# Kernel tuning notes

Hardware: AMD Instinct MI355X
Metric: run time of the kernel (lower is better)

The kernel has to match this reference:

```python
import jax, jax.numpy as jnp
import numpy as np

COUPLE_STRENGTH = 0.1
ITER_FISTA = 16
ITER_EIGENVAL = 20


def setup_inputs() -> dict:
    key = jax.random.key(0)
    k1, k2 = jax.random.split(key)
    # light field patches: (b, N, u, v, s, t, ch)
    x = jax.random.normal(k1, (8, 256, 5, 5, 4, 4, 3), dtype=jnp.float32)
    dim_signal = 5 * 5 * 4 * 4 * 3  # 1200
    dim_dict = 2 * dim_signal       # overcompleteness = 2 -> 2400
    D = jax.random.normal(k2, (dim_signal, dim_dict), dtype=jnp.float32)
    D = D / jnp.linalg.norm(D, axis=0, keepdims=True)  # UnitNorm(axis=0) constraint
    return {"x": x, "dictionary": D}


def _max_eigval(D):
    """von Mises power iteration for largest eigenvalue of D^T D."""
    v0 = jax.random.normal(jax.random.key(42), (D.shape[1],), dtype=D.dtype)
    v0 = v0 / jnp.linalg.norm(v0)

    def step(v, _):
        w = D.T @ (D @ v)
        n = jnp.linalg.norm(w)
        return w / n, n

    _, norms = jax.lax.scan(step, v0, None, length=ITER_EIGENVAL)
    return norms[-1]


def _soft_threshold(x, thr):
    return jnp.sign(x) * jnp.maximum(jnp.abs(x) - thr, 0.0)


def _sparse_code_fista(x2, D):
    """x2: (B, N, dim_signal); D: (dim_signal, dim_dict) -> codes (B, N, dim_dict)."""
    L = _max_eigval(D)            # Lipschitz constant of grad of 0.5*||Dz - x||^2
    thr = COUPLE_STRENGTH / L
    z0 = jnp.zeros(x2.shape[:-1] + (D.shape[1],), dtype=x2.dtype)
    carry0 = (z0, z0, jnp.float32(1.0))  # (z, y, t)

    def step(carry, _):
        z, y, t = carry
        recon = jnp.einsum('bnk,dk->bnd', y, D)             # (B,N,ds)
        grad = jnp.einsum('bnd,dk->bnk', recon - x2, D)     # (B,N,dd)
        z_new = _soft_threshold(y - grad / L, thr)
        t_new = 0.5 * (1.0 + jnp.sqrt(1.0 + 4.0 * t * t))
        y_new = z_new + ((t - 1.0) / t_new) * (z_new - z)   # Nesterov momentum
        return (z_new, y_new, t_new), None

    (z, _, _), _ = jax.lax.scan(step, carry0, None, length=ITER_FISTA)
    return z


def reference(x, dictionary):
    B, N, u, v, s, t, ch = x.shape
    x2 = x.reshape(B, N, u * v * s * t * ch)
    code = jax.lax.stop_gradient(_sparse_code_fista(x2, dictionary))
    recon = jnp.einsum('bnk,dk->bnd', code, dictionary)  # matmul(x, D, transpose_b=True)
    return recon.reshape(B, N, u, v, s, t, ch)
```

## Files before the change

kernel.cpp:

```cpp
#include <hip/hip_runtime.h>
#include <hip/hip_bf16.h>
#include <cmath>

#define DS 1200
#define DD 2400
#define MR 2048
#define KP 1216
#define NP1 1280
#define NG 2432
#define PPI 150

typedef __attribute__((ext_vector_type(8))) short s16x8;
typedef __attribute__((ext_vector_type(4))) float f32x4;

__device__ __forceinline__ float s2f(short s) {
    union { unsigned u; float f; } c;
    c.u = ((unsigned)(unsigned short)s) << 16;
    return c.f;
}
__device__ __forceinline__ short f2s(float f) {
    __hip_bfloat16 h = __float2bfloat16(f);
    return *reinterpret_cast<short*>(&h);
}
__device__ __forceinline__ float bf2f(__hip_bfloat16 h) { return __bfloat162float(h); }


__device__ __forceinline__ unsigned rotl32(unsigned x, int d) {
    return (x << d) | (x >> (32 - d));
}

__device__ void threefry2x32(unsigned k0, unsigned k1, unsigned x0, unsigned x1,
                             unsigned* o0, unsigned* o1) {
    unsigned ks0 = k0, ks1 = k1, ks2 = k0 ^ k1 ^ 0x1BD11BDAu;
    const int rotA[4] = {13, 15, 26, 6};
    const int rotB[4] = {17, 29, 16, 24};
    x0 += ks0; x1 += ks1;
    #pragma unroll
    for (int r = 0; r < 4; r++) { x0 += x1; x1 = rotl32(x1, rotA[r]); x1 ^= x0; }
    x0 += ks1; x1 += ks2 + 1u;
    #pragma unroll
    for (int r = 0; r < 4; r++) { x0 += x1; x1 = rotl32(x1, rotB[r]); x1 ^= x0; }
    x0 += ks2; x1 += ks0 + 2u;
    #pragma unroll
    for (int r = 0; r < 4; r++) { x0 += x1; x1 = rotl32(x1, rotA[r]); x1 ^= x0; }
    x0 += ks0; x1 += ks1 + 3u;
    #pragma unroll
    for (int r = 0; r < 4; r++) { x0 += x1; x1 = rotl32(x1, rotB[r]); x1 ^= x0; }
    x0 += ks1; x1 += ks2 + 4u;
    #pragma unroll
    for (int r = 0; r < 4; r++) { x0 += x1; x1 = rotl32(x1, rotA[r]); x1 ^= x0; }
    x0 += ks2; x1 += ks0 + 5u;
    *o0 = x0; *o1 = x1;
}

__device__ float erfinv_f32(float x) {
    float w = -logf((1.0f - x) * (1.0f + x));
    float p;
    if (w < 5.0f) {
        w -= 2.5f;
        p = 2.81022636e-08f;
        p = fmaf(p, w, 3.43273939e-07f);
        p = fmaf(p, w, -3.5233877e-06f);
        p = fmaf(p, w, -4.39150654e-06f);
        p = fmaf(p, w, 0.00021858087f);
        p = fmaf(p, w, -0.00125372503f);
        p = fmaf(p, w, -0.00417768164f);
        p = fmaf(p, w, 0.246640727f);
        p = fmaf(p, w, 1.50140941f);
    } else {
        w = sqrtf(w) - 3.0f;
        p = -0.000200214257f;
        p = fmaf(p, w, 0.000100950558f);
        p = fmaf(p, w, 0.00134934322f);
        p = fmaf(p, w, -0.00367342844f);
        p = fmaf(p, w, 0.00573950773f);
        p = fmaf(p, w, -0.0076224613f);
        p = fmaf(p, w, 0.00943887047f);
        p = fmaf(p, w, 1.00167406f);
        p = fmaf(p, w, 2.83297682f);
    }
    return p * x;
}

__device__ float bits_to_normal(unsigned bits) {
    unsigned fb = (bits >> 9) | 0x3F800000u;
    float u01 = __uint_as_float(fb) - 1.0f;
    const float lo = -0.99999994f;
    float u = u01 * 2.0f + lo;
    u = fmaxf(lo, u);
    return 1.41421356237f * erfinv_f32(u);
}

__global__ void k_init(float* __restrict__ w0, float* __restrict__ w1,
                       float* __restrict__ part) {
    int tid = threadIdx.x;
    for (int i = tid; i < 21 * PPI; i += 256) part[i] = 0.0f;
    if (tid < 32) {
        w0[2400 + tid] = 0.0f;
        w1[2400 + tid] = 0.0f;
    }
    __shared__ float red[256];
    float local2 = 0.0f;
    for (int p = tid; p < DS; p += 256) {
        unsigned r0, r1;
        threefry2x32(0u, 42u, (unsigned)p, (unsigned)(DS + p), &r0, &r1);
        float n0 = bits_to_normal(r0);
        float n1 = bits_to_normal(r1);
        w0[p] = n0;
        w0[DS + p] = n1;
        local2 += n0 * n0 + n1 * n1;
    }
    red[tid] = local2;
    __syncthreads();
    for (int s = 128; s > 0; s >>= 1) {
        if (tid < s) red[tid] += red[tid + s];
        __syncthreads();
    }
    if (tid == 0) part[0] = red[0];
}

__global__ __launch_bounds__(1024) void k_gmv(const short* __restrict__ Grm,
                                              const float* __restrict__ win,
                                              const float* __restrict__ partin,
                                              float* __restrict__ wout,
                                              float* __restrict__ partout) {
    float s2 = 0.0f;
    for (int i = 0; i < PPI; i++) s2 += partin[i];
    float rn = 1.0f / sqrtf(s2);
    int wave = threadIdx.x >> 6, lane = threadIdx.x & 63;
    int row = blockIdx.x * 16 + wave;
    const s16x8* gh = (const s16x8*)(Grm + (size_t)row * NG);
    const float4* w4 = (const float4*)win;
    float acc = 0.0f;
    #pragma unroll
    for (int i = 0; i < 5; i++) {
        int c = lane + i * 64;
        if (c < 304) {
            s16x8 h = gh[c];
            float4 wa = w4[c * 2], wb = w4[c * 2 + 1];
            acc += s2f(h[0]) * wa.x + s2f(h[1]) * wa.y;
            acc += s2f(h[2]) * wa.z + s2f(h[3]) * wa.w;
            acc += s2f(h[4]) * wb.x + s2f(h[5]) * wb.y;
            acc += s2f(h[6]) * wb.z + s2f(h[7]) * wb.w;
        }
    }
    #pragma unroll
    for (int off = 32; off > 0; off >>= 1) acc += __shfl_xor(acc, off, 64);
    __shared__ float red[16];
    if (lane == 0) {
        float val = acc * rn;
        wout[row] = val;
        red[wave] = val * val;
    }
    __syncthreads();
    if (threadIdx.x == 0) {
        float s = 0.0f;
        #pragma unroll
        for (int i = 0; i < 16; i++) s += red[i];
        partout[blockIdx.x] = s;
    }
}

__global__ void k_fin(const float* __restrict__ part20, float* __restrict__ scal) {
    if (threadIdx.x == 0) {
        float s = 0.0f;
        for (int i = 0; i < PPI; i++) s += part20[i];
        float L = sqrtf(s);
        scal[0] = L;
        scal[1] = 1.0f / L;
        scal[2] = 0.1f / L;
    }
}

__global__ void k_makeD(const float* __restrict__ D, short* __restrict__ Dp) {
    int p = blockIdx.x * 256 + threadIdx.x;
    if (p >= NP1 * NG) return;
    int tile = p >> 10, win = p & 1023;
    int row = win >> 3, e = win & 7;
    int mt = tile / (NG >> 3), ct = tile % (NG >> 3);
    int d = mt * 128 + row, n = ct * 8 + e;
    float v = (d < DS && n < DD) ? D[(size_t)d * DD + n] : 0.0f;
    Dp[p] = f2s(v);
}

__global__ void k_makeX(const float* __restrict__ x,
                        short* __restrict__ Xhi, short* __restrict__ Xlo) {
    int p = blockIdx.x * 256 + threadIdx.x;
    if (p >= MR * KP) return;
    int tile = p >> 10, win = p & 1023;
    int row = win >> 3, e = win & 7;
    int mt = tile / (KP >> 3), ct = tile % (KP >> 3);
    int m = mt * 128 + row, k = ct * 8 + e;
    float v = (k < DS) ? x[(size_t)m * DS + k] : 0.0f;
    short h = f2s(v);
    Xhi[p] = h;
    Xlo[p] = f2s(v - s2f(h));
}

__global__ void k_makeDt(const float* __restrict__ D,
                         short* __restrict__ Dthi, short* __restrict__ Dtlo) {
    __shared__ float t[32][33];
    int bc = blockIdx.x * 32;
    int bk = blockIdx.y * 32;
    int tx = threadIdx.x & 31, ty = threadIdx.x >> 5;
    for (int i = ty; i < 32; i += 8) {
        int k = bk + i, c = bc + tx;
        t[i][tx] = (k < DS && c < DD) ? D[(size_t)k * DD + c] : 0.0f;
    }
    __syncthreads();
    for (int i = ty; i < 32; i += 8) {
        int c = bc + i, k = bk + tx;
        float v = t[tx][i];
        short h = f2s(v);
        size_t po = ((size_t)(c >> 7) * (KP >> 3) + (k >> 3)) * 1024 +
                    ((c & 127) << 3) + (k & 7);
        Dthi[po] = h;
        Dtlo[po] = f2s(v - s2f(h));
    }
}

__global__ void k_zero_s(s16x8* __restrict__ p, int n8) {
    int i = blockIdx.x * blockDim.x + threadIdx.x;
    if (i < n8) {
        s16x8 z = {0, 0, 0, 0, 0, 0, 0, 0};
        p[i] = z;
    }
}

__device__ __forceinline__ void gload16(const void* g, void* l) {
    __builtin_amdgcn_global_load_lds(
        (const __attribute__((address_space(1))) unsigned int*)g,
        (__attribute__((address_space(3))) unsigned int*)l, 16, 0, 0);
}

template <int EPI, bool SPLIT>
__global__ __launch_bounds__(256) void mfma_gemm(
    const short* __restrict__ Ah, const short* __restrict__ Al, int CA,
    const short* __restrict__ Bh, const short* __restrict__ Bl, int CB,
    int K, int swz,
    const float* __restrict__ XDc, const float* __restrict__ scal, float mom,
    short* __restrict__ Ynew, short* __restrict__ Zst,
    short* __restrict__ Gp, short* __restrict__ Grm,
    float* __restrict__ Out) {
    constexpr int BK = SPLIT ? 32 : 64;
    constexpr int ASZ = 128 * BK;
    constexpr int RNDS = (128 * (BK / 8)) / 256;
    constexpr int ALO_ = SPLIT ? ASZ : 0;
    constexpr int BHO_ = SPLIT ? 2 * ASZ : ASZ;
    constexpr int BLO_ = 3 * ASZ;
    __shared__ __align__(16) short lds[2 * 16384];

    const int tid = threadIdx.x;
    const int w = tid >> 6, lane = tid & 63;
    const int fm = lane & 15, kg = lane >> 4;
    const int wr = w >> 1, wc = w & 1;

    int bx, by;
    if (swz) {
        int q = gridDim.x >> 3;
        int s = (blockIdx.x & 7) * q + (blockIdx.x >> 3);
        bx = s >> 4; by = s & 15;
    } else { bx = blockIdx.x; by = blockIdx.y; }
    const int m0 = by * 128, n0 = bx * 128;

    f32x4 acc[4][4];
    #pragma unroll
    for (int g = 0; g < 4; ++g)
        #pragma unroll
        for (int h = 0; h < 4; ++h) acc[g][h] = f32x4{0.f, 0.f, 0.f, 0.f};

    float invL = 0.0f, thr = 0.0f;
    if (EPI == 2) { invL = scal[1]; thr = scal[2]; }

    const int soff0 = ((tid >> 7) << 10) + ((tid & 127) << 3);
    const size_t Abase = (size_t)m0 * CA + soff0;
    const size_t Bbase = (size_t)n0 * CB + soff0;

    const int nk = K / BK;

    auto STAGE = [&](int t, int cur) {
        const int kk = t * (BK * 128 / 8) * 8;
        short* bp = &lds[cur * 16384];
        #pragma unroll
        for (int r = 0; r < RNDS; ++r) {
            const int lo = (r * 256 + w * 64) * 8;
            gload16(Ah + Abase + kk + r * 2048, bp + lo);
            if constexpr (SPLIT) gload16(Al + Abase + kk + r * 2048, bp + ALO_ + lo);
            gload16(Bh + Bbase + kk + r * 2048, bp + BHO_ + lo);
            if constexpr (SPLIT) gload16(Bl + Bbase + kk + r * 2048, bp + BLO_ + lo);
        }
    };

    STAGE(0, 0);

    for (int t = 0; t < nk; ++t) {
        __syncthreads();
        if (t + 1 < nk) STAGE(t + 1, (t + 1) & 1);
        const short* bs = &lds[(t & 1) * 16384];

        #pragma unroll
        for (int ks = 0; ks < BK / 32; ++ks) {
            const int c = ks * 4 + kg;
            s16x8 a[4], b[4];
            #pragma unroll
            for (int g = 0; g < 4; ++g)
                a[g] = *(const s16x8*)&bs[c * 1024 + (wr * 64 + g * 16 + fm) * 8];
            #pragma unroll
            for (int h = 0; h < 4; ++h)
                b[h] = *(const s16x8*)&bs[BHO_ + c * 1024 + (wc * 64 + h * 16 + fm) * 8];
            if constexpr (SPLIT) {
                s16x8 a2[4], b2[4];
                #pragma unroll
                for (int g = 0; g < 4; ++g)
                    a2[g] = *(const s16x8*)&bs[ALO_ + c * 1024 + (wr * 64 + g * 16 + fm) * 8];
                #pragma unroll
                for (int h = 0; h < 4; ++h)
                    b2[h] = *(const s16x8*)&bs[BLO_ + c * 1024 + (wc * 64 + h * 16 + fm) * 8];
                #pragma unroll
                for (int g = 0; g < 4; ++g)
                    #pragma unroll
                    for (int h = 0; h < 4; ++h) {
                        acc[g][h] = __builtin_amdgcn_mfma_f32_16x16x32_bf16(a[g], b[h], acc[g][h], 0, 0, 0);
                        acc[g][h] = __builtin_amdgcn_mfma_f32_16x16x32_bf16(a[g], b2[h], acc[g][h], 0, 0, 0);
                        acc[g][h] = __builtin_amdgcn_mfma_f32_16x16x32_bf16(a2[g], b[h], acc[g][h], 0, 0, 0);
                    }
            } else {
                #pragma unroll
                for (int g = 0; g < 4; ++g)
                    #pragma unroll
                    for (int h = 0; h < 4; ++h)
                        acc[g][h] = __builtin_amdgcn_mfma_f32_16x16x32_bf16(a[g], b[h], acc[g][h], 0, 0, 0);
            }
        }
    }

    #pragma unroll
    for (int g = 0; g < 4; ++g) {
        #pragma unroll
        for (int h = 0; h < 4; ++h) {
            #pragma unroll
            for (int j = 0; j < 4; ++j) {
                int m = m0 + wr * 64 + g * 16 + kg * 4 + j;
                int n = n0 + wc * 64 + h * 16 + fm;
                float v = acc[g][h][j];
                if (EPI == 0) {
                    if (n < DS) Out[(size_t)m * DS + n] = v;
                } else if (EPI == 2) {
                    size_t o = (size_t)m * NG + n;
                    size_t pz = (size_t)(m & ~127) * NG + ((n >> 3) << 10) +
                                ((m & 127) << 3) + (n & 7);
                    float grad = v - XDc[o];
                    float yold = s2f(Ah[pz]);
                    float zold = s2f(Zst[pz]);
                    float gs = yold - grad * invL;
                    float az = fabsf(gs) - thr;
                    float zn = (az > 0.0f) ? copysignf(az, gs) : 0.0f;
                    float yn = zn + mom * (zn - zold);
                    Zst[pz] = f2s(zn);
                    Ynew[pz] = f2s(yn);
                } else if (EPI == 3) {
                    Out[(size_t)m * NG + n] = v;
                } else {
                    size_t pz = (size_t)(m & ~127) * NG + ((n >> 3) << 10) +
                                ((m & 127) << 3) + (n & 7);
                    short hv = f2s(v);
                    Gp[pz] = hv;
                    Grm[(size_t)m * NG + n] = hv;
                }
            }
        }
    }
}

extern "C" void kernel_launch(void* const* d_in, const int* in_sizes, int n_in,
                              void* d_out, int out_size, void* d_ws, size_t ws_size,
                              hipStream_t stream) {
    const float* x = (const float*)d_in[0];
    const float* D = (const float*)d_in[1];
    float* out = (float*)d_out;

    char* wsb = (char*)d_ws;
    float* w0 = (float*)wsb;
    float* w1 = w0 + 2432;
    float* part = w1 + 2432;
    float* scal = part + 3200;

    char* p = wsb + 65536;
    short* Dp   = (short*)p; p += (size_t)NP1 * NG * 2;
    short* Dthi = (short*)p; p += (size_t)NG * KP * 2;
    short* Dtlo = (short*)p; p += (size_t)NG * KP * 2;
    short* Xhi  = (short*)p; p += (size_t)MR * KP * 2;
    short* Xlo  = (short*)p; p += (size_t)MR * KP * 2;
    short* Gp   = (short*)p; p += (size_t)NG * NG * 2;
    short* Grm  = (short*)p; p += (size_t)NG * NG * 2;
    float* XD   = (float*)p; p += (size_t)MR * NG * 4;
    short* Y0p  = (short*)p; p += (size_t)MR * NG * 2;
    short* Zp   = (short*)p; p += (size_t)MR * NG * 2;
    short* Y1p  = (short*)p; p += (size_t)MR * NG * 2;

    k_makeD<<<(NP1 * NG + 255) / 256, 256, 0, stream>>>(D, Dp);
    k_makeDt<<<dim3(NG / 32, KP / 32), 256, 0, stream>>>(D, Dthi, Dtlo);
    k_makeX<<<(MR * KP + 255) / 256, 256, 0, stream>>>(x, Xhi, Xlo);

    mfma_gemm<4, true><<<dim3(NG / 128, NG / 128), 256, 0, stream>>>(
        Dthi, Dtlo, KP, Dthi, Dtlo, KP, KP, 0,
        nullptr, nullptr, 0.0f, nullptr, nullptr, Gp, Grm, nullptr);

    mfma_gemm<3, true><<<dim3(304), 256, 0, stream>>>(
        Xhi, Xlo, KP, Dthi, Dtlo, KP, KP, 1,
        nullptr, nullptr, 0.0f, nullptr, nullptr, nullptr, nullptr, XD);

    k_init<<<1, 256, 0, stream>>>(w0, w1, part);
    for (int j = 0; j < 20; j++) {
        const float* win = (j & 1) ? w1 : w0;
        float* wout = (j & 1) ? w0 : w1;
        k_gmv<<<PPI, 1024, 0, stream>>>(Grm, win, part + j * PPI, wout,
                                        part + (j + 1) * PPI);
    }
    k_fin<<<1, 64, 0, stream>>>(part + 20 * PPI, scal);

    {
        int n8 = 2 * MR * NG / 8;
        k_zero_s<<<(n8 + 255) / 256, 256, 0, stream>>>((s16x8*)Y0p, n8);
    }

    float t = 1.0f;
    for (int i = 0; i < 16; i++) {
        float tn = 0.5f * (1.0f + sqrtf(1.0f + 4.0f * t * t));
        float mom = (t - 1.0f) / tn;
        t = tn;
        short* Yc = (i & 1) ? Y1p : Y0p;
        short* Yn = (i & 1) ? Y0p : Y1p;
        mfma_gemm<2, false><<<dim3(304), 256, 0, stream>>>(
            Yc, nullptr, NG, Gp, nullptr, NG, NG, 1,
            XD, scal, mom, Yn, Zp, nullptr, nullptr, nullptr);
    }

    mfma_gemm<0, false><<<dim3(160), 256, 0, stream>>>(
        Zp, nullptr, NG, Dp, nullptr, NG, NG, 1,
        nullptr, nullptr, 0.0f, nullptr, nullptr, nullptr, nullptr, out);
}
```

Baseline: 954.9 us.

## Shrink GEMM tiles to 64x128 and peel first FISTA iteration

The shared MFMA GEMM now uses 64-row by 128-column tiles with a K-step of 32 and a smaller LDS footprint, and declares a minimum of 4 blocks per SM. This doubles the grid to 608 blocks for better occupancy and CU fill on a 256-CU part. The first FISTA iteration, where y is zero, is replaced by an elementwise kernel that applies soft-thresholding to XD directly. That saves one Gram GEMM and the zeroing kernel. In exchange, each block reuses less data, so more global and LDS traffic is needed per MFMA.

Result: no change. 940.5 us (-1.5%).

```diff
diff --git a/kernel.cpp b/kernel.cpp
--- a/kernel.cpp
+++ b/kernel.cpp
@@ -22,7 +22,6 @@
     __hip_bfloat16 h = __float2bfloat16(f);
     return *reinterpret_cast<short*>(&h);
 }
-__device__ __forceinline__ float bf2f(__hip_bfloat16 h) { return __bfloat162float(h); }
 
 
 __device__ __forceinline__ unsigned rotl32(unsigned x, int d) {
@@ -219,12 +218,31 @@
     }
 }
 
-__global__ void k_zero_s(s16x8* __restrict__ p, int n8) {
-    int i = blockIdx.x * blockDim.x + threadIdx.x;
-    if (i < n8) {
-        s16x8 z = {0, 0, 0, 0, 0, 0, 0, 0};
-        p[i] = z;
-    }
+__global__ void k_fista0(const float* __restrict__ XD, const float* __restrict__ scal,
+                         short* __restrict__ Z, short* __restrict__ Y) {
+    int i = blockIdx.x * 256 + threadIdx.x;
+    if (i >= MR * NG / 8) return;
+    float invL = scal[1], thr = scal[2];
+    int e0 = i * 8;
+    int band = e0 / (128 * NG);
+    int rem = e0 - band * (128 * NG);
+    int tile = rem >> 10;
+    int row = (rem & 1023) >> 3;
+    int m = band * 128 + row;
+    int n = tile * 8;
+    const float4* xp = (const float4*)(XD + (size_t)m * NG + n);
+    float4 v0 = xp[0], v1 = xp[1];
+    float vs[8] = {v0.x, v0.y, v0.z, v0.w, v1.x, v1.y, v1.z, v1.w};
+    s16x8 zs;
+    #pragma unroll
+    for (int k = 0; k < 8; k++) {
+        float gs = vs[k] * invL;
+        float az = fabsf(gs) - thr;
+        float zn = (az > 0.0f) ? copysignf(az, gs) : 0.0f;
+        zs[k] = f2s(zn);
+    }
+    ((s16x8*)Z)[i] = zs;
+    ((s16x8*)Y)[i] = zs;
 }
 
 __device__ __forceinline__ void gload16(const void* g, void* l) {
@@ -234,7 +252,7 @@
 }
 
 template <int EPI, bool SPLIT>
-__global__ __launch_bounds__(256) void mfma_gemm(
+__global__ __launch_bounds__(256, 4) void mfma_gemm(
     const short* __restrict__ Ah, const short* __restrict__ Al, int CA,
     const short* __restrict__ Bh, const short* __restrict__ Bl, int CB,
     int K, int swz,
@@ -242,13 +260,11 @@
     short* __restrict__ Ynew, short* __restrict__ Zst,
     short* __restrict__ Gp, short* __restrict__ Grm,
     float* __restrict__ Out) {
-    constexpr int BK = SPLIT ? 32 : 64;
-    constexpr int ASZ = 128 * BK;
-    constexpr int RNDS = (128 * (BK / 8)) / 256;
-    constexpr int ALO_ = SPLIT ? ASZ : 0;
-    constexpr int BHO_ = SPLIT ? 2 * ASZ : ASZ;
-    constexpr int BLO_ = 3 * ASZ;
-    __shared__ __align__(16) short lds[2 * 16384];
+    constexpr int ALO = 2048;
+    constexpr int BHO = SPLIT ? 4096 : 2048;
+    constexpr int BLO = 8192;
+    constexpr int BUF = SPLIT ? 12288 : 6144;
+    __shared__ __align__(16) short lds[2 * BUF];
 
     const int tid = threadIdx.x;
     const int w = tid >> 6, lane = tid & 63;
@@ -259,35 +275,35 @@
     if (swz) {
         int q = gridDim.x >> 3;
         int s = (blockIdx.x & 7) * q + (blockIdx.x >> 3);
-        bx = s >> 4; by = s & 15;
+        by = s & 31; bx = s >> 5;
     } else { bx = blockIdx.x; by = blockIdx.y; }
-    const int m0 = by * 128, n0 = bx * 128;
-
-    f32x4 acc[4][4];
-    #pragma unroll
-    for (int g = 0; g < 4; ++g)
+    const int m0 = by * 64, n0 = bx * 128;
+
+    f32x4 acc[2][4];
+    #pragma unroll
+    for (int g = 0; g < 2; ++g)
         #pragma unroll
         for (int h = 0; h < 4; ++h) acc[g][h] = f32x4{0.f, 0.f, 0.f, 0.f};
 
     float invL = 0.0f, thr = 0.0f;
     if (EPI == 2) { invL = scal[1]; thr = scal[2]; }
 
-    const int soff0 = ((tid >> 7) << 10) + ((tid & 127) << 3);
-    const size_t Abase = (size_t)m0 * CA + soff0;
-    const size_t Bbase = (size_t)n0 * CB + soff0;
-
-    const int nk = K / BK;
+    const int half = (m0 >> 6) & 1;
+    const size_t Aoff = (size_t)(m0 & ~127) * CA + w * 1024 + half * 512 + lane * 8;
+    const size_t Boff = (size_t)n0 * CB + w * 512 + lane * 8;
+
+    const int nk = K >> 5;
 
     auto STAGE = [&](int t, int cur) {
-        const int kk = t * (BK * 128 / 8) * 8;
-        short* bp = &lds[cur * 16384];
-        #pragma unroll
-        for (int r = 0; r < RNDS; ++r) {
-            const int lo = (r * 256 + w * 64) * 8;
-            gload16(Ah + Abase + kk + r * 2048, bp + lo);
-            if constexpr (SPLIT) gload16(Al + Abase + kk + r * 2048, bp + ALO_ + lo);
-            gload16(Bh + Bbase + kk + r * 2048, bp + BHO_ + lo);
-            if constexpr (SPLIT) gload16(Bl + Bbase + kk + r * 2048, bp + BLO_ + lo);
+        const int kk = t << 12;
+        short* bp = &lds[cur * BUF];
+        gload16(Ah + Aoff + kk, bp + w * 512);
+        gload16(Bh + Boff + kk, bp + BHO + w * 512);
+        gload16(Bh + Boff + kk + 2048, bp + BHO + 2048 + w * 512);
+        if constexpr (SPLIT) {
+            gload16(Al + Aoff + kk, bp + ALO + w * 512);
+            gload16(Bl + Boff + kk, bp + BLO + w * 512);
+            gload16(Bl + Boff + kk + 2048, bp + BLO + 2048 + w * 512);
         }
     };
 
@@ -296,51 +312,47 @@
     for (int t = 0; t < nk; ++t) {
         __syncthreads();
         if (t + 1 < nk) STAGE(t + 1, (t + 1) & 1);
-        const short* bs = &lds[(t & 1) * 16384];
-
+        const short* bs = &lds[(t & 1) * BUF];
+
+        s16x8 a[2], b[4];
         #pragma unroll
-        for (int ks = 0; ks < BK / 32; ++ks) {
-            const int c = ks * 4 + kg;
-            s16x8 a[4], b[4];
+        for (int g = 0; g < 2; ++g)
+            a[g] = *(const s16x8*)&bs[kg * 512 + (wr * 32 + g * 16 + fm) * 8];
+        #pragma unroll
+        for (int h = 0; h < 4; ++h)
+            b[h] = *(const s16x8*)&bs[BHO + kg * 1024 + (wc * 64 + h * 16 + fm) * 8];
+        if constexpr (SPLIT) {
+            s16x8 a2[2], b2[4];
             #pragma unroll
-            for (int g = 0; g < 4; ++g)
-                a[g] = *(const s16x8*)&bs[c * 1024 + (wr * 64 + g * 16 + fm) * 8];
+            for (int g = 0; g < 2; ++g)
+                a2[g] = *(const s16x8*)&bs[ALO + kg * 512 + (wr * 32 + g * 16 + fm) * 8];
             #pragma unroll
             for (int h = 0; h < 4; ++h)
-                b[h] = *(const s16x8*)&bs[BHO_ + c * 1024 + (wc * 64 + h * 16 + fm) * 8];
-            if constexpr (SPLIT) {
-                s16x8 a2[4], b2[4];
+                b2[h] = *(const s16x8*)&bs[BLO + kg * 1024 + (wc * 64 + h * 16 + fm) * 8];
+            #pragma unroll
+            for (int g = 0; g < 2; ++g)
                 #pragma unroll
-                for (int g = 0; g < 4; ++g)
-                    a2[g] = *(const s16x8*)&bs[ALO_ + c * 1024 + (wr * 64 + g * 16 + fm) * 8];
+                for (int h = 0; h < 4; ++h) {
+                    acc[g][h] = __builtin_amdgcn_mfma_f32_16x16x32_bf16(a[g], b[h], acc[g][h], 0, 0, 0);
+                    acc[g][h] = __builtin_amdgcn_mfma_f32_16x16x32_bf16(a[g], b2[h], acc[g][h], 0, 0, 0);
+                    acc[g][h] = __builtin_amdgcn_mfma_f32_16x16x32_bf16(a2[g], b[h], acc[g][h], 0, 0, 0);
+                }
+        } else {
+            #pragma unroll
+            for (int g = 0; g < 2; ++g)
                 #pragma unroll
                 for (int h = 0; h < 4; ++h)
-                    b2[h] = *(const s16x8*)&bs[BLO_ + c * 1024 + (wc * 64 + h * 16 + fm) * 8];
-                #pragma unroll
-                for (int g = 0; g < 4; ++g)
-                    #pragma unroll
-                    for (int h = 0; h < 4; ++h) {
-                        acc[g][h] = __builtin_amdgcn_mfma_f32_16x16x32_bf16(a[g], b[h], acc[g][h], 0, 0, 0);
-                        acc[g][h] = __builtin_amdgcn_mfma_f32_16x16x32_bf16(a[g], b2[h], acc[g][h], 0, 0, 0);
-                        acc[g][h] = __builtin_amdgcn_mfma_f32_16x16x32_bf16(a2[g], b[h], acc[g][h], 0, 0, 0);
-                    }
-            } else {
-                #pragma unroll
-                for (int g = 0; g < 4; ++g)
-                    #pragma unroll
-                    for (int h = 0; h < 4; ++h)
-                        acc[g][h] = __builtin_amdgcn_mfma_f32_16x16x32_bf16(a[g], b[h], acc[g][h], 0, 0, 0);
-            }
+                    acc[g][h] = __builtin_amdgcn_mfma_f32_16x16x32_bf16(a[g], b[h], acc[g][h], 0, 0, 0);
         }
     }
 
     #pragma unroll
-    for (int g = 0; g < 4; ++g) {
+    for (int g = 0; g < 2; ++g) {
         #pragma unroll
         for (int h = 0; h < 4; ++h) {
             #pragma unroll
             for (int j = 0; j < 4; ++j) {
-                int m = m0 + wr * 64 + g * 16 + kg * 4 + j;
+                int m = m0 + wr * 32 + g * 16 + kg * 4 + j;
                 int n = n0 + wc * 64 + h * 16 + fm;
                 float v = acc[g][h][j];
                 if (EPI == 0) {
@@ -394,19 +406,19 @@
     short* Gp   = (short*)p; p += (size_t)NG * NG * 2;
     short* Grm  = (short*)p; p += (size_t)NG * NG * 2;
     float* XD   = (float*)p; p += (size_t)MR * NG * 4;
-    short* Y0p  = (short*)p; p += (size_t)MR * NG * 2;
+    short* Ya   = (short*)p; p += (size_t)MR * NG * 2;
+    short* Yb   = (short*)p; p += (size_t)MR * NG * 2;
     short* Zp   = (short*)p; p += (size_t)MR * NG * 2;
-    short* Y1p  = (short*)p; p += (size_t)MR * NG * 2;
 
     k_makeD<<<(NP1 * NG + 255) / 256, 256, 0, stream>>>(D, Dp);
     k_makeDt<<<dim3(NG / 32, KP / 32), 256, 0, stream>>>(D, Dthi, Dtlo);
     k_makeX<<<(MR * KP + 255) / 256, 256, 0, stream>>>(x, Xhi, Xlo);
 
-    mfma_gemm<4, true><<<dim3(NG / 128, NG / 128), 256, 0, stream>>>(
+    mfma_gemm<4, true><<<dim3(NG / 128, NG / 64), 256, 0, stream>>>(
         Dthi, Dtlo, KP, Dthi, Dtlo, KP, KP, 0,
         nullptr, nullptr, 0.0f, nullptr, nullptr, Gp, Grm, nullptr);
 
-    mfma_gemm<3, true><<<dim3(304), 256, 0, stream>>>(
+    mfma_gemm<3, true><<<dim3(608), 256, 0, stream>>>(
         Xhi, Xlo, KP, Dthi, Dtlo, KP, KP, 1,
         nullptr, nullptr, 0.0f, nullptr, nullptr, nullptr, nullptr, XD);
 
@@ -419,24 +431,21 @@
     }
     k_fin<<<1, 64, 0, stream>>>(part + 20 * PPI, scal);
 
-    {
-        int n8 = 2 * MR * NG / 8;
-        k_zero_s<<<(n8 + 255) / 256, 256, 0, stream>>>((s16x8*)Y0p, n8);
-    }
-
-    float t = 1.0f;
-    for (int i = 0; i < 16; i++) {
+    k_fista0<<<(MR * NG / 8 + 255) / 256, 256, 0, stream>>>(XD, scal, Zp, Ya);
+
+    float t = 1.6180339887f;
+    for (int i = 1; i < 16; i++) {
         float tn = 0.5f * (1.0f + sqrtf(1.0f + 4.0f * t * t));
         float mom = (t - 1.0f) / tn;
         t = tn;
-        short* Yc = (i & 1) ? Y1p : Y0p;
-        short* Yn = (i & 1) ? Y0p : Y1p;
-        mfma_gemm<2, false><<<dim3(304), 256, 0, stream>>>(
+        short* Yc = (i & 1) ? Ya : Yb;
+        short* Yn = (i & 1) ? Yb : Ya;
+        mfma_gemm<2, false><<<dim3(608), 256, 0, stream>>>(
             Yc, nullptr, NG, Gp, nullptr, NG, NG, 1,
             XD, scal, mom, Yn, Zp, nullptr, nullptr, nullptr);
     }
 
-    mfma_gemm<0, false><<<dim3(160), 256, 0, stream>>>(
+    mfma_gemm<0, false><<<dim3(320), 256, 0, stream>>>(
         Zp, nullptr, NG, Dp, nullptr, NG, NG, 1,
         nullptr, nullptr, 0.0f, nullptr, nullptr, nullptr, nullptr, out);
 }
```
